# Kernel optimization log

Measured on AMD Instinct MI355X. Metric: run time of the kernel, lower is better.

Reference implementation:

```python
import jax, jax.numpy as jnp
import numpy as np

N_NODES = 100000
N_EDGES = 1600000
NFEAT = 128
NHID = 128
NCLASS = 40


def gcn_conv(x, W, b, src, dst, n_nodes):
    """PyG-style GCNConv: x' = D^{-1/2}(A+I)D^{-1/2} (x W) + b."""
    h = x @ W  # [N, out]
    loop = jnp.arange(n_nodes, dtype=src.dtype)
    s = jnp.concatenate([src, loop])  # add self-loops
    d = jnp.concatenate([dst, loop])
    deg = jax.ops.segment_sum(jnp.ones_like(s, dtype=h.dtype), d, num_segments=n_nodes)
    dinv = jnp.where(deg > 0, jax.lax.rsqrt(deg), 0.0)
    norm = dinv[s] * dinv[d]  # [E+N]
    msg = h[s] * norm[:, None]  # gather + scale
    out = jax.ops.segment_sum(msg, d, num_segments=n_nodes)  # scatter-add
    return out + b


def setup_inputs() -> dict:
    key = jax.random.key(0)
    ks = jax.random.split(key, 6)
    x = jax.random.normal(ks[0], (N_NODES, NFEAT), dtype=jnp.float32)
    edge_index = jax.random.randint(ks[1], (2, N_EDGES), 0, N_NODES, dtype=jnp.int64)
    sc1 = 1.0 / np.sqrt(NFEAT)
    sc2 = 1.0 / np.sqrt(NHID)
    W1 = jax.random.normal(ks[2], (NFEAT, NHID), dtype=jnp.float32) * sc1
    b1 = jnp.zeros((NHID,), dtype=jnp.float32)
    Wm = jax.random.normal(ks[3], (NHID, NHID), dtype=jnp.float32) * sc2
    bm = jnp.zeros((NHID,), dtype=jnp.float32)
    W2 = jax.random.normal(ks[4], (NHID, NCLASS), dtype=jnp.float32) * sc2
    b2 = jnp.zeros((NCLASS,), dtype=jnp.float32)
    return {"x": x, "edge_index": edge_index, "W1": W1, "b1": b1,
            "Wm": Wm, "bm": bm, "W2": W2, "b2": b2}


def reference(x, edge_index, W1, b1, Wm, bm, W2, b2):
    # StandGCNX forward, eval mode (dropout = identity)
    src, dst = edge_index[0], edge_index[1]
    n = x.shape[0]
    h = jax.nn.relu(gcn_conv(x, W1, b1, src, dst, n))
    h = jax.nn.relu(gcn_conv(h, Wm, bm, src, dst, n))
    out = gcn_conv(h, W2, b2, src, dst, n)
    return out
```

## Files before the change

kernel.cpp:

```cpp
#include <hip/hip_runtime.h>
#include <hip/hip_bf16.h>

typedef __attribute__((ext_vector_type(8))) short bf16x8;
typedef __attribute__((ext_vector_type(4))) float f32x4;

__device__ __forceinline__ ushort bf16rne(float f) {
    uint u = __float_as_uint(f);
    return (ushort)((u + 0x7fffu + ((u >> 16) & 1u)) >> 16);
}
__device__ __forceinline__ void unpack2(uint p, float& a, float& b) {
    a = __uint_as_float(p << 16);
    b = __uint_as_float(p & 0xffff0000u);
}


__global__ __launch_bounds__(256) void k_pre1(const float* __restrict__ W1,
                                              const float* __restrict__ Wm,
                                              const float* __restrict__ W2,
                                              ushort* __restrict__ w1t,
                                              ushort* __restrict__ wmt,
                                              ushort* __restrict__ w2t,
                                              const int* __restrict__ dst,
                                              int* __restrict__ bcnt, int E) {
    __shared__ int hist[512];
    int b = blockIdx.x;
    int t = threadIdx.x;
    if (b < 152) {
        if (b < 64) {
            int i = b * 256 + t; int k = i >> 7, n = i & 127;
            w1t[n * 128 + k] = bf16rne(W1[k * 128 + n]);
        } else if (b < 128) {
            int i = (b - 64) * 256 + t; int k = i >> 7, n = i & 127;
            wmt[n * 128 + k] = bf16rne(Wm[k * 128 + n]);
        } else {
            int i = (b - 128) * 256 + t;
            if (i < 6144) {
                int n = i >> 7, k = i & 127;
                w2t[n * 128 + k] = (n < 40) ? bf16rne(W2[k * 40 + n]) : (ushort)0;
            }
        }
        return;
    }
    hist[t] = 0; hist[t + 256] = 0;
    __syncthreads();
    int off = (b - 152) * 4096;
    int cnt = min(4096, E - off);
    for (int i = t; i < cnt; i += 256) atomicAdd(&hist[dst[off + i] >> 8], 1);
    __syncthreads();
    if (hist[t]) atomicAdd(&bcnt[t], hist[t]);
    if (hist[t + 256]) atomicAdd(&bcnt[t + 256], hist[t + 256]);
}

__global__ void k_bscan(const int* __restrict__ bcnt, int* __restrict__ bbase,
                        int* __restrict__ bcur, int nbuck) {
    __shared__ int s[512];
    int t = threadIdx.x;
    s[t] = (t < nbuck) ? bcnt[t] : 0;
    __syncthreads();
    for (int d = 1; d < 512; d <<= 1) {
        int u = (t >= d) ? s[t - d] : 0;
        __syncthreads();
        if (t >= d) s[t] += u;
        __syncthreads();
    }
    int excl = (t == 0) ? 0 : s[t - 1];
    bbase[t] = excl;
    if (t < nbuck) bcur[t] = excl;
    if (t == 511) bbase[512] = s[511];
}


__global__ __launch_bounds__(256) void k_pack_gemm(const int* __restrict__ src,
                                                   const int* __restrict__ dst,
                                                   int* __restrict__ bcur,
                                                   uint* __restrict__ pairbuf,
                                                   int E, int nbuck, int ntile,
                                                   const float* __restrict__ A,
                                                   const ushort* __restrict__ Wt,
                                                   ushort* __restrict__ C, int M) {
    __shared__ int hist[512];
    __shared__ int scn[512];
    __shared__ int cur[512];
    __shared__ int gbase[512];
    __shared__ uint sorted[4096];
    int t = threadIdx.x;
    if ((int)blockIdx.x >= ntile) {
        int blk = blockIdx.x - ntile;
        int wave = t >> 6, lane = t & 63;
        int m16 = lane & 15, quad = lane >> 4;
        int rowA = blk * 64 + wave * 16 + m16;
        int rA = min(rowA, M - 1);
        const float4* A4 = (const float4*)A;

        f32x4 acc[8];
#pragma unroll
        for (int i = 0; i < 8; i++) acc[i] = (f32x4){0.f, 0.f, 0.f, 0.f};
#pragma unroll
        for (int it = 0; it < 4; it++) {
            float4 f0 = A4[(size_t)rA * 32 + 8 * it + 2 * quad];
            float4 f1 = A4[(size_t)rA * 32 + 8 * it + 2 * quad + 1];
            bf16x8 af;
            af[0] = (short)bf16rne(f0.x); af[1] = (short)bf16rne(f0.y);
            af[2] = (short)bf16rne(f0.z); af[3] = (short)bf16rne(f0.w);
            af[4] = (short)bf16rne(f1.x); af[5] = (short)bf16rne(f1.y);
            af[6] = (short)bf16rne(f1.z); af[7] = (short)bf16rne(f1.w);
#pragma unroll
            for (int nt = 0; nt < 8; nt++) {
                bf16x8 bfr = *(const bf16x8*)(Wt + (size_t)(nt * 16 + m16) * 128 + it * 32 + quad * 8);
                acc[nt] = __builtin_amdgcn_mfma_f32_16x16x32_bf16(af, bfr, acc[nt], 0, 0, 0);
            }
        }
        int rowBase = blk * 64 + wave * 16 + quad * 4;
#pragma unroll
        for (int nt = 0; nt < 8; nt++) {
            int col = nt * 16 + m16;
#pragma unroll
            for (int r = 0; r < 4; r++) {
                int row = rowBase + r;
                if (row < M) C[(size_t)row * 128 + col] = bf16rne(acc[nt][r]);
            }
        }
        return;
    }
    int off = blockIdx.x * 4096;
    int cnt = min(4096, E - off);
    hist[t] = 0; hist[t + 256] = 0;
    __syncthreads();
    for (int i = t; i < cnt; i += 256) {
        int b = dst[off + i] >> 8;
        atomicAdd(&hist[b], 1);
    }
    __syncthreads();
    scn[t] = hist[t]; scn[t + 256] = hist[t + 256];
    __syncthreads();
    for (int d = 1; d < 256; d <<= 1) {
        int u0 = (t >= d) ? scn[t - d] : 0;
        int u1 = (t >= d) ? scn[256 + t - d] : 0;
        __syncthreads();
        if (t >= d) { scn[t] += u0; scn[256 + t] += u1; }
        __syncthreads();
    }
    int tot0 = scn[255];
    scn[256 + t] += tot0;
    __syncthreads();
    cur[t] = (t == 0) ? 0 : scn[t - 1];
    cur[t + 256] = scn[t + 255];
    if (t < nbuck && hist[t] > 0) gbase[t] = atomicAdd(&bcur[t], hist[t]);
    int t2 = t + 256;
    if (t2 < nbuck && hist[t2] > 0) gbase[t2] = atomicAdd(&bcur[t2], hist[t2]);
    __syncthreads();
    for (int i = t; i < cnt; i += 256) {
        int d = dst[off + i];
        int s = src[off + i];
        int b = d >> 8;
        int pos = atomicAdd(&cur[b], 1);
        sorted[pos] = ((uint)(d & 255) << 24) | (uint)s;
    }
    __syncthreads();
    int wid = t >> 6, lane = t & 63;
    for (int b = wid; b < nbuck; b += 4) {
        int n = hist[b];
        if (n == 0) continue;
        int ls = (b == 0) ? 0 : scn[b - 1];
        int gb = gbase[b];
        for (int j = lane; j < n; j += 64)
            pairbuf[gb + j] = sorted[ls + j];
    }
}

#define CSR_CAP 5632
__global__ __launch_bounds__(256) void k_csrbuild(const uint* __restrict__ pairbuf,
                                                  const int* __restrict__ bbase,
                                                  int* __restrict__ rowptr,
                                                  float* __restrict__ dinv,
                                                  int* __restrict__ csr,
                                                  int N, int nbuck) {
    __shared__ int lhist[256];
    __shared__ int scn[256];
    __shared__ int lcur[256];
    __shared__ int lcsr[CSR_CAP];
    int b = blockIdx.x;
    int base = b << 8;
    int nn = min(256, N - base);
    int lo = bbase[b], hi = bbase[b + 1];
    int cnt = hi - lo;
    int t = threadIdx.x;
    lhist[t] = 0;
    __syncthreads();
    for (int i = t; i < cnt; i += 256) atomicAdd(&lhist[pairbuf[lo + i] >> 24], 1);
    __syncthreads();
    int mydeg = lhist[t];
    scn[t] = mydeg;
    __syncthreads();
    for (int d = 1; d < 256; d <<= 1) {
        int u = (t >= d) ? scn[t - d] : 0;
        __syncthreads();
        if (t >= d) scn[t] += u;
        __syncthreads();
    }
    int excl = (t == 0) ? 0 : scn[t - 1];
    lcur[t] = excl;
    if (t < nn) {
        rowptr[base + t] = lo + excl;
        dinv[base + t] = rsqrtf((float)(mydeg + 1));
    }
    if (b == nbuck - 1 && t == 0) rowptr[N] = hi;
    __syncthreads();
    if (cnt <= CSR_CAP) {
        for (int i = t; i < cnt; i += 256) {
            uint p = pairbuf[lo + i];
            int pos = atomicAdd(&lcur[p >> 24], 1);
            lcsr[pos] = (int)(p & 0xFFFFFFu);
        }
        __syncthreads();
        for (int i = t; i < cnt; i += 256) csr[lo + i] = lcsr[i];
    } else {
        for (int i = t; i < cnt; i += 256) {
            uint p = pairbuf[lo + i];
            int pos = lo + atomicAdd(&lcur[p >> 24], 1);
            csr[pos] = (int)(p & 0xFFFFFFu);
        }
    }
}


template <int NT, bool EDGE_W>
__device__ __forceinline__ void fused_agg_gemm(const ushort* __restrict__ g,
                                               const float* __restrict__ dinv,
                                               const int* __restrict__ rowptr,
                                               const int* __restrict__ csr,
                                               const float* __restrict__ bias,
                                               const ushort* __restrict__ Wt,
                                               ushort* __restrict__ C,
                                               int M, int ccols) {
    __shared__ ushort hs[32][136];
    __shared__ int nextNode;
    int t = threadIdx.x;
    if (t == 0) nextNode = 0;
    int l = t & 15;
    const uint4* g16 = (const uint4*)g;
    float4 bb0 = ((const float4*)bias)[2 * l];
    float4 bb1 = ((const float4*)bias)[2 * l + 1];
    __syncthreads();

    for (;;) {
        int idx = 0;
        if (l == 0) idx = atomicAdd(&nextNode, 1);
        idx = __shfl(idx, (t & 63) & ~15, 64);
        if (idx >= 32) break;
        int node = blockIdx.x * 32 + idx;
        int nd = min(node, M - 1);
        float dn = dinv[nd];
        float a[8];
        {
            uint4 p = g16[(size_t)nd * 16 + l];
            float u, v;
            if (EDGE_W) {
                unpack2(p.x, u, v); a[0] = u * dn; a[1] = v * dn;
                unpack2(p.y, u, v); a[2] = u * dn; a[3] = v * dn;
                unpack2(p.z, u, v); a[4] = u * dn; a[5] = v * dn;
                unpack2(p.w, u, v); a[6] = u * dn; a[7] = v * dn;
            } else {
                unpack2(p.x, a[0], a[1]); unpack2(p.y, a[2], a[3]);
                unpack2(p.z, a[4], a[5]); unpack2(p.w, a[6], a[7]);
            }
        }
        int e0 = rowptr[nd], e1 = rowptr[nd + 1];
        int e = e0;
        for (; e + 4 <= e1; e += 4) {
            int s0 = csr[e], s1 = csr[e + 1], s2 = csr[e + 2], s3 = csr[e + 3];
            float w0 = 1.f, w1 = 1.f, w2 = 1.f, w3 = 1.f;
            if (EDGE_W) { w0 = dinv[s0]; w1 = dinv[s1]; w2 = dinv[s2]; w3 = dinv[s3]; }
            uint4 p0 = g16[(size_t)s0 * 16 + l];
            uint4 p1 = g16[(size_t)s1 * 16 + l];
            uint4 p2 = g16[(size_t)s2 * 16 + l];
            uint4 p3 = g16[(size_t)s3 * 16 + l];
            float u, v;
            if (EDGE_W) {
                unpack2(p0.x, u, v); a[0] += u * w0; a[1] += v * w0;
                unpack2(p0.y, u, v); a[2] += u * w0; a[3] += v * w0;
                unpack2(p0.z, u, v); a[4] += u * w0; a[5] += v * w0;
                unpack2(p0.w, u, v); a[6] += u * w0; a[7] += v * w0;
                unpack2(p1.x, u, v); a[0] += u * w1; a[1] += v * w1;
                unpack2(p1.y, u, v); a[2] += u * w1; a[3] += v * w1;
                unpack2(p1.z, u, v); a[4] += u * w1; a[5] += v * w1;
                unpack2(p1.w, u, v); a[6] += u * w1; a[7] += v * w1;
                unpack2(p2.x, u, v); a[0] += u * w2; a[1] += v * w2;
                unpack2(p2.y, u, v); a[2] += u * w2; a[3] += v * w2;
                unpack2(p2.z, u, v); a[4] += u * w2; a[5] += v * w2;
                unpack2(p2.w, u, v); a[6] += u * w2; a[7] += v * w2;
                unpack2(p3.x, u, v); a[0] += u * w3; a[1] += v * w3;
                unpack2(p3.y, u, v); a[2] += u * w3; a[3] += v * w3;
                unpack2(p3.z, u, v); a[4] += u * w3; a[5] += v * w3;
                unpack2(p3.w, u, v); a[6] += u * w3; a[7] += v * w3;
            } else {
                unpack2(p0.x, u, v); a[0] += u; a[1] += v;
                unpack2(p0.y, u, v); a[2] += u; a[3] += v;
                unpack2(p0.z, u, v); a[4] += u; a[5] += v;
                unpack2(p0.w, u, v); a[6] += u; a[7] += v;
                unpack2(p1.x, u, v); a[0] += u; a[1] += v;
                unpack2(p1.y, u, v); a[2] += u; a[3] += v;
                unpack2(p1.z, u, v); a[4] += u; a[5] += v;
                unpack2(p1.w, u, v); a[6] += u; a[7] += v;
                unpack2(p2.x, u, v); a[0] += u; a[1] += v;
                unpack2(p2.y, u, v); a[2] += u; a[3] += v;
                unpack2(p2.z, u, v); a[4] += u; a[5] += v;
                unpack2(p2.w, u, v); a[6] += u; a[7] += v;
                unpack2(p3.x, u, v); a[0] += u; a[1] += v;
                unpack2(p3.y, u, v); a[2] += u; a[3] += v;
                unpack2(p3.z, u, v); a[4] += u; a[5] += v;
                unpack2(p3.w, u, v); a[6] += u; a[7] += v;
            }
        }
        for (; e < e1; e++) {
            int s = csr[e];
            float w = EDGE_W ? dinv[s] : 1.f;
            uint4 p = g16[(size_t)s * 16 + l];
            float u, v;
            unpack2(p.x, u, v); a[0] += u * w; a[1] += v * w;
            unpack2(p.y, u, v); a[2] += u * w; a[3] += v * w;
            unpack2(p.z, u, v); a[4] += u * w; a[5] += v * w;
            unpack2(p.w, u, v); a[6] += u * w; a[7] += v * w;
        }
        float o0 = fmaxf(a[0] * dn + bb0.x, 0.f);
        float o1 = fmaxf(a[1] * dn + bb0.y, 0.f);
        float o2 = fmaxf(a[2] * dn + bb0.z, 0.f);
        float o3 = fmaxf(a[3] * dn + bb0.w, 0.f);
        float o4 = fmaxf(a[4] * dn + bb1.x, 0.f);
        float o5 = fmaxf(a[5] * dn + bb1.y, 0.f);
        float o6 = fmaxf(a[6] * dn + bb1.z, 0.f);
        float o7 = fmaxf(a[7] * dn + bb1.w, 0.f);
        uint4 qv;
        qv.x = (uint)bf16rne(o0) | ((uint)bf16rne(o1) << 16);
        qv.y = (uint)bf16rne(o2) | ((uint)bf16rne(o3) << 16);
        qv.z = (uint)bf16rne(o4) | ((uint)bf16rne(o5) << 16);
        qv.w = (uint)bf16rne(o6) | ((uint)bf16rne(o7) << 16);
        *(uint4*)&hs[idx][l * 8] = qv;
    }
    __syncthreads();

    int wave = t >> 6, lane = t & 63;
    int m16 = lane & 15, quad = lane >> 4;
    int rowHalf = wave & 1;
    int ntHalf = wave >> 1;
    constexpr int NTH = (NT + 1) / 2;
    int ntStart = ntHalf * NTH;
    int ntEnd = ntHalf ? NT : NTH;

    f32x4 acc[NTH];
#pragma unroll
    for (int i = 0; i < NTH; i++) acc[i] = (f32x4){0.f, 0.f, 0.f, 0.f};
#pragma unroll
    for (int it = 0; it < 4; it++) {
        bf16x8 af = *(const bf16x8*)&hs[rowHalf * 16 + m16][it * 32 + quad * 8];
        for (int nt = ntStart; nt < ntEnd; nt++) {
            bf16x8 bfr = *(const bf16x8*)(Wt + (size_t)(nt * 16 + m16) * 128 + it * 32 + quad * 8);
            acc[nt - ntStart] = __builtin_amdgcn_mfma_f32_16x16x32_bf16(af, bfr, acc[nt - ntStart], 0, 0, 0);
        }
    }
    int rowBase = blockIdx.x * 32 + rowHalf * 16 + quad * 4;
    float dnv[4];
#pragma unroll
    for (int r = 0; r < 4; r++) dnv[r] = dinv[min(rowBase + r, M - 1)];
    for (int nt = ntStart; nt < ntEnd; nt++) {
        int col = nt * 16 + m16;
        if (col >= ccols) continue;
#pragma unroll
        for (int r = 0; r < 4; r++) {
            int row = rowBase + r;
            if (row < M) C[(size_t)row * ccols + col] = bf16rne(acc[nt - ntStart][r] * dnv[r]);
        }
    }
}

__global__ __launch_bounds__(256) void k_fusedA(const ushort* __restrict__ g,
                                                const float* __restrict__ dinv,
                                                const int* __restrict__ rowptr,
                                                const int* __restrict__ csr,
                                                const float* __restrict__ bias,
                                                const ushort* __restrict__ Wt,
                                                ushort* __restrict__ C, int M) {
    fused_agg_gemm<8, true>(g, dinv, rowptr, csr, bias, Wt, C, M, 128);
}

__global__ __launch_bounds__(256) void k_fusedB(const ushort* __restrict__ g,
                                                const float* __restrict__ dinv,
                                                const int* __restrict__ rowptr,
                                                const int* __restrict__ csr,
                                                const float* __restrict__ bias,
                                                const ushort* __restrict__ Wt,
                                                ushort* __restrict__ C, int M) {
    fused_agg_gemm<3, false>(g, dinv, rowptr, csr, bias, Wt, C, M, 40);
}


__global__ __launch_bounds__(256) void k_agg40_b(const ushort* __restrict__ g3,
                                                 const float* __restrict__ dinv,
                                                 const int* __restrict__ rowptr,
                                                 const int* __restrict__ csr,
                                                 const float* __restrict__ bias,
                                                 float* __restrict__ out, int N) {
    int t = threadIdx.x;
    if (t >= 250) return;
    int grp = t / 10;
    int l = t - grp * 10;
    int node = blockIdx.x * 25 + grp;
    if (node >= N) return;
    const uint2* gp = (const uint2*)g3;
    float dn = dinv[node];
    float a0, a1, a2, a3;
    {
        uint2 p = gp[(size_t)node * 10 + l];
        unpack2(p.x, a0, a1);
        unpack2(p.y, a2, a3);
    }
    int e0 = rowptr[node], e1 = rowptr[node + 1];
    int e = e0;
    for (; e + 4 <= e1; e += 4) {
        int s0 = csr[e], s1 = csr[e + 1], s2 = csr[e + 2], s3 = csr[e + 3];
        uint2 p0 = gp[(size_t)s0 * 10 + l];
        uint2 p1 = gp[(size_t)s1 * 10 + l];
        uint2 p2 = gp[(size_t)s2 * 10 + l];
        uint2 p3 = gp[(size_t)s3 * 10 + l];
        float u, v;
        unpack2(p0.x, u, v); a0 += u; a1 += v;
        unpack2(p0.y, u, v); a2 += u; a3 += v;
        unpack2(p1.x, u, v); a0 += u; a1 += v;
        unpack2(p1.y, u, v); a2 += u; a3 += v;
        unpack2(p2.x, u, v); a0 += u; a1 += v;
        unpack2(p2.y, u, v); a2 += u; a3 += v;
        unpack2(p3.x, u, v); a0 += u; a1 += v;
        unpack2(p3.y, u, v); a2 += u; a3 += v;
    }
    for (; e < e1; e++) {
        int s = csr[e];
        uint2 p = gp[(size_t)s * 10 + l];
        float u, v;
        unpack2(p.x, u, v); a0 += u; a1 += v;
        unpack2(p.y, u, v); a2 += u; a3 += v;
    }
    float4 bb = ((const float4*)bias)[l];
    float4 o;
    o.x = a0 * dn + bb.x;
    o.y = a1 * dn + bb.y;
    o.z = a2 * dn + bb.z;
    o.w = a3 * dn + bb.w;
    ((float4*)out)[(size_t)node * 10 + l] = o;
}


extern "C" void kernel_launch(void* const* d_in, const int* in_sizes, int n_in,
                              void* d_out, int out_size, void* d_ws, size_t ws_size,
                              hipStream_t stream) {
    const float* x  = (const float*)d_in[0];
    const int* eidx = (const int*)d_in[1];
    const float* W1 = (const float*)d_in[2];
    const float* b1 = (const float*)d_in[3];
    const float* Wm = (const float*)d_in[4];
    const float* bm = (const float*)d_in[5];
    const float* W2 = (const float*)d_in[6];
    const float* b2 = (const float*)d_in[7];
    float* out = (float*)d_out;

    int N = in_sizes[0] / 128;
    int E = in_sizes[1] / 2;
    const int* src = eidx;
    const int* dst = eidx + E;
    int nbuck = (N + 255) >> 8;
    int ntile = (E + 4095) / 4096;

    char* ws = (char*)d_ws;
    size_t off = 0;
    auto alloc = [&](size_t bytes) -> void* {
        void* p = ws + off;
        off += (bytes + 255) & ~(size_t)255;
        return p;
    };
    float*  dinv    = (float*)alloc((size_t)N * 4);
    int*    rowptr  = (int*)alloc(((size_t)N + 1) * 4);
    int*    csr     = (int*)alloc((size_t)E * 4);
    uint*   pairbuf = (uint*)alloc((size_t)E * 4);
    int*    bcnt    = (int*)alloc(512 * 4);
    int*    bbase   = (int*)alloc(513 * 4);
    int*    bcur    = (int*)alloc(512 * 4);
    ushort* w1t     = (ushort*)alloc(128 * 128 * 2);
    ushort* wmt     = (ushort*)alloc(128 * 128 * 2);
    ushort* w2t     = (ushort*)alloc(48 * 128 * 2);
    ushort* gbuf    = (ushort*)alloc((size_t)N * 128 * 2);
    ushort* gbuf2   = (ushort*)alloc((size_t)N * 128 * 2);
    ushort* g3      = (ushort*)alloc((size_t)N * 40 * 2);

    int gblk64 = (N + 63) / 64;
    int gblk32 = (N + 31) / 32;

    hipMemsetAsync(bcnt, 0, 512 * 4, stream);
    k_pre1<<<152 + ntile, 256, 0, stream>>>(W1, Wm, W2, w1t, wmt, w2t, dst, bcnt, E);
    k_bscan<<<1, 512, 0, stream>>>(bcnt, bbase, bcur, nbuck);
    k_pack_gemm<<<ntile + gblk64, 256, 0, stream>>>(src, dst, bcur, pairbuf, E, nbuck,
                                                    ntile, x, w1t, gbuf, N);
    k_csrbuild<<<nbuck, 256, 0, stream>>>(pairbuf, bbase, rowptr, dinv, csr, N, nbuck);
    k_fusedA<<<gblk32, 256, 0, stream>>>(gbuf, dinv, rowptr, csr, b1, wmt, gbuf2, N);
    k_fusedB<<<gblk32, 256, 0, stream>>>(gbuf2, dinv, rowptr, csr, bm, w2t, g3, N);
    k_agg40_b<<<(N + 24) / 25, 256, 0, stream>>>(g3, dinv, rowptr, csr, b2, out, N);
}
```

Measured before the change: 368.3 us.

## Split fused aggregation+GEMM kernels into separate aggregation and MFMA GEMM kernels

Replaces the two fused aggregate-then-GEMM kernels with four kernels. Two are plain per-node gather aggregations writing a bf16 hidden buffer, and two are standalone MFMA GEMMs that read that buffer. This removes the LDS staging, the atomic work-stealing loop and the block-wide sync that tied aggregation to the GEMM, and allows simpler, higher-occupancy kernels. The cost is an extra 25.6MB bf16 intermediate written and read twice, plus two more kernel launches.

```diff
diff --git a/kernel.cpp b/kernel.cpp
--- a/kernel.cpp
+++ b/kernel.cpp
@@ -224,173 +224,176 @@
 }
 
 
-template <int NT, bool EDGE_W>
-__device__ __forceinline__ void fused_agg_gemm(const ushort* __restrict__ g,
-                                               const float* __restrict__ dinv,
-                                               const int* __restrict__ rowptr,
-                                               const int* __restrict__ csr,
-                                               const float* __restrict__ bias,
-                                               const ushort* __restrict__ Wt,
-                                               ushort* __restrict__ C,
-                                               int M, int ccols) {
-    __shared__ ushort hs[32][136];
-    __shared__ int nextNode;
-    int t = threadIdx.x;
-    if (t == 0) nextNode = 0;
+template <bool EDGE_W>
+__device__ __forceinline__ void agg128_body(const ushort* __restrict__ g,
+                                            const float* __restrict__ dinv,
+                                            const int* __restrict__ rowptr,
+                                            const int* __restrict__ csr,
+                                            const float* __restrict__ bias,
+                                            ushort* __restrict__ hout, int N) {
+    int t = threadIdx.x;
+    int grp = t >> 4;
     int l = t & 15;
+    int node = blockIdx.x * 16 + grp;
+    if (node >= N) return;
     const uint4* g16 = (const uint4*)g;
-    float4 bb0 = ((const float4*)bias)[2 * l];
-    float4 bb1 = ((const float4*)bias)[2 * l + 1];
-    __syncthreads();
-
-    for (;;) {
-        int idx = 0;
-        if (l == 0) idx = atomicAdd(&nextNode, 1);
-        idx = __shfl(idx, (t & 63) & ~15, 64);
-        if (idx >= 32) break;
-        int node = blockIdx.x * 32 + idx;
-        int nd = min(node, M - 1);
-        float dn = dinv[nd];
-        float a[8];
-        {
-            uint4 p = g16[(size_t)nd * 16 + l];
-            float u, v;
-            if (EDGE_W) {
-                unpack2(p.x, u, v); a[0] = u * dn; a[1] = v * dn;
-                unpack2(p.y, u, v); a[2] = u * dn; a[3] = v * dn;
-                unpack2(p.z, u, v); a[4] = u * dn; a[5] = v * dn;
-                unpack2(p.w, u, v); a[6] = u * dn; a[7] = v * dn;
-            } else {
-                unpack2(p.x, a[0], a[1]); unpack2(p.y, a[2], a[3]);
-                unpack2(p.z, a[4], a[5]); unpack2(p.w, a[6], a[7]);
-            }
-        }
-        int e0 = rowptr[nd], e1 = rowptr[nd + 1];
-        int e = e0;
-        for (; e + 4 <= e1; e += 4) {
-            int s0 = csr[e], s1 = csr[e + 1], s2 = csr[e + 2], s3 = csr[e + 3];
-            float w0 = 1.f, w1 = 1.f, w2 = 1.f, w3 = 1.f;
-            if (EDGE_W) { w0 = dinv[s0]; w1 = dinv[s1]; w2 = dinv[s2]; w3 = dinv[s3]; }
-            uint4 p0 = g16[(size_t)s0 * 16 + l];
-            uint4 p1 = g16[(size_t)s1 * 16 + l];
-            uint4 p2 = g16[(size_t)s2 * 16 + l];
-            uint4 p3 = g16[(size_t)s3 * 16 + l];
-            float u, v;
-            if (EDGE_W) {
-                unpack2(p0.x, u, v); a[0] += u * w0; a[1] += v * w0;
-                unpack2(p0.y, u, v); a[2] += u * w0; a[3] += v * w0;
-                unpack2(p0.z, u, v); a[4] += u * w0; a[5] += v * w0;
-                unpack2(p0.w, u, v); a[6] += u * w0; a[7] += v * w0;
-                unpack2(p1.x, u, v); a[0] += u * w1; a[1] += v * w1;
-                unpack2(p1.y, u, v); a[2] += u * w1; a[3] += v * w1;
-                unpack2(p1.z, u, v); a[4] += u * w1; a[5] += v * w1;
-                unpack2(p1.w, u, v); a[6] += u * w1; a[7] += v * w1;
-                unpack2(p2.x, u, v); a[0] += u * w2; a[1] += v * w2;
-                unpack2(p2.y, u, v); a[2] += u * w2; a[3] += v * w2;
-                unpack2(p2.z, u, v); a[4] += u * w2; a[5] += v * w2;
-                unpack2(p2.w, u, v); a[6] += u * w2; a[7] += v * w2;
-                unpack2(p3.x, u, v); a[0] += u * w3; a[1] += v * w3;
-                unpack2(p3.y, u, v); a[2] += u * w3; a[3] += v * w3;
-                unpack2(p3.z, u, v); a[4] += u * w3; a[5] += v * w3;
-                unpack2(p3.w, u, v); a[6] += u * w3; a[7] += v * w3;
-            } else {
-                unpack2(p0.x, u, v); a[0] += u; a[1] += v;
-                unpack2(p0.y, u, v); a[2] += u; a[3] += v;
-                unpack2(p0.z, u, v); a[4] += u; a[5] += v;
-                unpack2(p0.w, u, v); a[6] += u; a[7] += v;
-                unpack2(p1.x, u, v); a[0] += u; a[1] += v;
-                unpack2(p1.y, u, v); a[2] += u; a[3] += v;
-                unpack2(p1.z, u, v); a[4] += u; a[5] += v;
-                unpack2(p1.w, u, v); a[6] += u; a[7] += v;
-                unpack2(p2.x, u, v); a[0] += u; a[1] += v;
-                unpack2(p2.y, u, v); a[2] += u; a[3] += v;
-                unpack2(p2.z, u, v); a[4] += u; a[5] += v;
-                unpack2(p2.w, u, v); a[6] += u; a[7] += v;
-                unpack2(p3.x, u, v); a[0] += u; a[1] += v;
-                unpack2(p3.y, u, v); a[2] += u; a[3] += v;
-                unpack2(p3.z, u, v); a[4] += u; a[5] += v;
-                unpack2(p3.w, u, v); a[6] += u; a[7] += v;
-            }
-        }
-        for (; e < e1; e++) {
-            int s = csr[e];
-            float w = EDGE_W ? dinv[s] : 1.f;
-            uint4 p = g16[(size_t)s * 16 + l];
-            float u, v;
-            unpack2(p.x, u, v); a[0] += u * w; a[1] += v * w;
-            unpack2(p.y, u, v); a[2] += u * w; a[3] += v * w;
-            unpack2(p.z, u, v); a[4] += u * w; a[5] += v * w;
-            unpack2(p.w, u, v); a[6] += u * w; a[7] += v * w;
-        }
-        float o0 = fmaxf(a[0] * dn + bb0.x, 0.f);
-        float o1 = fmaxf(a[1] * dn + bb0.y, 0.f);
-        float o2 = fmaxf(a[2] * dn + bb0.z, 0.f);
-        float o3 = fmaxf(a[3] * dn + bb0.w, 0.f);
-        float o4 = fmaxf(a[4] * dn + bb1.x, 0.f);
-        float o5 = fmaxf(a[5] * dn + bb1.y, 0.f);
-        float o6 = fmaxf(a[6] * dn + bb1.z, 0.f);
-        float o7 = fmaxf(a[7] * dn + bb1.w, 0.f);
-        uint4 qv;
-        qv.x = (uint)bf16rne(o0) | ((uint)bf16rne(o1) << 16);
-        qv.y = (uint)bf16rne(o2) | ((uint)bf16rne(o3) << 16);
-        qv.z = (uint)bf16rne(o4) | ((uint)bf16rne(o5) << 16);
-        qv.w = (uint)bf16rne(o6) | ((uint)bf16rne(o7) << 16);
-        *(uint4*)&hs[idx][l * 8] = qv;
-    }
-    __syncthreads();
-
+    float dn = dinv[node];
+    float a[8];
+    {
+        uint4 p = g16[(size_t)node * 16 + l];
+        float u, v;
+        if (EDGE_W) {
+            unpack2(p.x, u, v); a[0] = u * dn; a[1] = v * dn;
+            unpack2(p.y, u, v); a[2] = u * dn; a[3] = v * dn;
+            unpack2(p.z, u, v); a[4] = u * dn; a[5] = v * dn;
+            unpack2(p.w, u, v); a[6] = u * dn; a[7] = v * dn;
+        } else {
+            unpack2(p.x, a[0], a[1]); unpack2(p.y, a[2], a[3]);
+            unpack2(p.z, a[4], a[5]); unpack2(p.w, a[6], a[7]);
+        }
+    }
+    int e0 = rowptr[node], e1 = rowptr[node + 1];
+    int e = e0;
+    for (; e + 4 <= e1; e += 4) {
+        int s0 = csr[e], s1 = csr[e + 1], s2 = csr[e + 2], s3 = csr[e + 3];
+        float w0 = 1.f, w1 = 1.f, w2 = 1.f, w3 = 1.f;
+        if (EDGE_W) { w0 = dinv[s0]; w1 = dinv[s1]; w2 = dinv[s2]; w3 = dinv[s3]; }
+        uint4 p0 = g16[(size_t)s0 * 16 + l];
+        uint4 p1 = g16[(size_t)s1 * 16 + l];
+        uint4 p2 = g16[(size_t)s2 * 16 + l];
+        uint4 p3 = g16[(size_t)s3 * 16 + l];
+        float u, v;
+        if (EDGE_W) {
+            unpack2(p0.x, u, v); a[0] += u * w0; a[1] += v * w0;
+            unpack2(p0.y, u, v); a[2] += u * w0; a[3] += v * w0;
+            unpack2(p0.z, u, v); a[4] += u * w0; a[5] += v * w0;
+            unpack2(p0.w, u, v); a[6] += u * w0; a[7] += v * w0;
+            unpack2(p1.x, u, v); a[0] += u * w1; a[1] += v * w1;
+            unpack2(p1.y, u, v); a[2] += u * w1; a[3] += v * w1;
+            unpack2(p1.z, u, v); a[4] += u * w1; a[5] += v * w1;
+            unpack2(p1.w, u, v); a[6] += u * w1; a[7] += v * w1;
+            unpack2(p2.x, u, v); a[0] += u * w2; a[1] += v * w2;
+            unpack2(p2.y, u, v); a[2] += u * w2; a[3] += v * w2;
+            unpack2(p2.z, u, v); a[4] += u * w2; a[5] += v * w2;
+            unpack2(p2.w, u, v); a[6] += u * w2; a[7] += v * w2;
+            unpack2(p3.x, u, v); a[0] += u * w3; a[1] += v * w3;
+            unpack2(p3.y, u, v); a[2] += u * w3; a[3] += v * w3;
+            unpack2(p3.z, u, v); a[4] += u * w3; a[5] += v * w3;
+            unpack2(p3.w, u, v); a[6] += u * w3; a[7] += v * w3;
+        } else {
+            unpack2(p0.x, u, v); a[0] += u; a[1] += v;
+            unpack2(p0.y, u, v); a[2] += u; a[3] += v;
+            unpack2(p0.z, u, v); a[4] += u; a[5] += v;
+            unpack2(p0.w, u, v); a[6] += u; a[7] += v;
+            unpack2(p1.x, u, v); a[0] += u; a[1] += v;
+            unpack2(p1.y, u, v); a[2] += u; a[3] += v;
+            unpack2(p1.z, u, v); a[4] += u; a[5] += v;
+            unpack2(p1.w, u, v); a[6] += u; a[7] += v;
+            unpack2(p2.x, u, v); a[0] += u; a[1] += v;
+            unpack2(p2.y, u, v); a[2] += u; a[3] += v;
+            unpack2(p2.z, u, v); a[4] += u; a[5] += v;
+            unpack2(p2.w, u, v); a[6] += u; a[7] += v;
+            unpack2(p3.x, u, v); a[0] += u; a[1] += v;
+            unpack2(p3.y, u, v); a[2] += u; a[3] += v;
+            unpack2(p3.z, u, v); a[4] += u; a[5] += v;
+            unpack2(p3.w, u, v); a[6] += u; a[7] += v;
+        }
+    }
+    for (; e < e1; e++) {
+        int s = csr[e];
+        float w = EDGE_W ? dinv[s] : 1.f;
+        uint4 p = g16[(size_t)s * 16 + l];
+        float u, v;
+        unpack2(p.x, u, v); a[0] += u * w; a[1] += v * w;
+        unpack2(p.y, u, v); a[2] += u * w; a[3] += v * w;
+        unpack2(p.z, u, v); a[4] += u * w; a[5] += v * w;
+        unpack2(p.w, u, v); a[6] += u * w; a[7] += v * w;
+    }
+    float4 b0 = ((const float4*)bias)[2 * l];
+    float4 b1 = ((const float4*)bias)[2 * l + 1];
+    float o[8];
+    o[0] = fmaxf(a[0] * dn + b0.x, 0.f); o[1] = fmaxf(a[1] * dn + b0.y, 0.f);
+    o[2] = fmaxf(a[2] * dn + b0.z, 0.f); o[3] = fmaxf(a[3] * dn + b0.w, 0.f);
+    o[4] = fmaxf(a[4] * dn + b1.x, 0.f); o[5] = fmaxf(a[5] * dn + b1.y, 0.f);
+    o[6] = fmaxf(a[6] * dn + b1.z, 0.f); o[7] = fmaxf(a[7] * dn + b1.w, 0.f);
+    uint4 q;
+    q.x = (uint)bf16rne(o[0]) | ((uint)bf16rne(o[1]) << 16);
+    q.y = (uint)bf16rne(o[2]) | ((uint)bf16rne(o[3]) << 16);
+    q.z = (uint)bf16rne(o[4]) | ((uint)bf16rne(o[5]) << 16);
+    q.w = (uint)bf16rne(o[6]) | ((uint)bf16rne(o[7]) << 16);
+    ((uint4*)hout)[(size_t)node * 16 + l] = q;
+}
+
+__global__ __launch_bounds__(256) void k_aggA(const ushort* __restrict__ g,
+                                              const float* __restrict__ dinv,
+                                              const int* __restrict__ rowptr,
+                                              const int* __restrict__ csr,
+                                              const float* __restrict__ bias,
+                                              ushort* __restrict__ hout, int N) {
+    agg128_body<true>(g, dinv, rowptr, csr, bias, hout, N);
+}
+
+__global__ __launch_bounds__(256) void k_aggB(const ushort* __restrict__ g,
+                                              const float* __restrict__ dinv,
+                                              const int* __restrict__ rowptr,
+                                              const int* __restrict__ csr,
+                                              const float* __restrict__ bias,
+                                              ushort* __restrict__ hout, int N) {
+    agg128_body<false>(g, dinv, rowptr, csr, bias, hout, N);
+}
+
+
+template <int NT>
+__device__ __forceinline__ void gemm_body(const ushort* __restrict__ A,
+                                          const ushort* __restrict__ Wt,
+                                          const float* __restrict__ dinv,
+                                          ushort* __restrict__ C, int M, int ccols) {
+    int t = threadIdx.x;
     int wave = t >> 6, lane = t & 63;
     int m16 = lane & 15, quad = lane >> 4;
-    int rowHalf = wave & 1;
-    int ntHalf = wave >> 1;
-    constexpr int NTH = (NT + 1) / 2;
-    int ntStart = ntHalf * NTH;
-    int ntEnd = ntHalf ? NT : NTH;
-
-    f32x4 acc[NTH];
-#pragma unroll
-    for (int i = 0; i < NTH; i++) acc[i] = (f32x4){0.f, 0.f, 0.f, 0.f};
+    int rowA = blockIdx.x * 64 + wave * 16 + m16;
+    int rA = min(rowA, M - 1);
+
+    f32x4 acc[NT];
+#pragma unroll
+    for (int i = 0; i < NT; i++) acc[i] = (f32x4){0.f, 0.f, 0.f, 0.f};
 #pragma unroll
     for (int it = 0; it < 4; it++) {
-        bf16x8 af = *(const bf16x8*)&hs[rowHalf * 16 + m16][it * 32 + quad * 8];
-        for (int nt = ntStart; nt < ntEnd; nt++) {
+        bf16x8 af = *(const bf16x8*)(A + (size_t)rA * 128 + it * 32 + quad * 8);
+#pragma unroll
+        for (int nt = 0; nt < NT; nt++) {
             bf16x8 bfr = *(const bf16x8*)(Wt + (size_t)(nt * 16 + m16) * 128 + it * 32 + quad * 8);
-            acc[nt - ntStart] = __builtin_amdgcn_mfma_f32_16x16x32_bf16(af, bfr, acc[nt - ntStart], 0, 0, 0);
-        }
-    }
-    int rowBase = blockIdx.x * 32 + rowHalf * 16 + quad * 4;
+            acc[nt] = __builtin_amdgcn_mfma_f32_16x16x32_bf16(af, bfr, acc[nt], 0, 0, 0);
+        }
+    }
+    int rowBase = blockIdx.x * 64 + wave * 16 + quad * 4;
     float dnv[4];
 #pragma unroll
     for (int r = 0; r < 4; r++) dnv[r] = dinv[min(rowBase + r, M - 1)];
-    for (int nt = ntStart; nt < ntEnd; nt++) {
+#pragma unroll
+    for (int nt = 0; nt < NT; nt++) {
         int col = nt * 16 + m16;
         if (col >= ccols) continue;
 #pragma unroll
         for (int r = 0; r < 4; r++) {
             int row = rowBase + r;
-            if (row < M) C[(size_t)row * ccols + col] = bf16rne(acc[nt - ntStart][r] * dnv[r]);
-        }
-    }
-}
-
-__global__ __launch_bounds__(256) void k_fusedA(const ushort* __restrict__ g,
-                                                const float* __restrict__ dinv,
-                                                const int* __restrict__ rowptr,
-                                                const int* __restrict__ csr,
-                                                const float* __restrict__ bias,
-                                                const ushort* __restrict__ Wt,
-                                                ushort* __restrict__ C, int M) {
-    fused_agg_gemm<8, true>(g, dinv, rowptr, csr, bias, Wt, C, M, 128);
-}
-
-__global__ __launch_bounds__(256) void k_fusedB(const ushort* __restrict__ g,
-                                                const float* __restrict__ dinv,
-                                                const int* __restrict__ rowptr,
-                                                const int* __restrict__ csr,
-                                                const float* __restrict__ bias,
-                                                const ushort* __restrict__ Wt,
-                                                ushort* __restrict__ C, int M) {
-    fused_agg_gemm<3, false>(g, dinv, rowptr, csr, bias, Wt, C, M, 40);
+            if (row < M) C[(size_t)row * ccols + col] = bf16rne(acc[nt][r] * dnv[r]);
+        }
+    }
+}
+
+__global__ __launch_bounds__(256) void k_gemm128s(const ushort* __restrict__ A,
+                                                  const ushort* __restrict__ Wt,
+                                                  const float* __restrict__ dinv,
+                                                  ushort* __restrict__ C, int M) {
+    gemm_body<8>(A, Wt, dinv, C, M, 128);
+}
+
+__global__ __launch_bounds__(256) void k_gemm40s(const ushort* __restrict__ A,
+                                                 const ushort* __restrict__ Wt,
+                                                 const float* __restrict__ dinv,
+                                                 ushort* __restrict__ C, int M) {
+    gemm_body<3>(A, Wt, dinv, C, M, 40);
 }
 
 
@@ -487,11 +490,12 @@
     ushort* wmt     = (ushort*)alloc(128 * 128 * 2);
     ushort* w2t     = (ushort*)alloc(48 * 128 * 2);
     ushort* gbuf    = (ushort*)alloc((size_t)N * 128 * 2);
+    ushort* hbuf    = (ushort*)alloc((size_t)N * 128 * 2);
     ushort* gbuf2   = (ushort*)alloc((size_t)N * 128 * 2);
     ushort* g3      = (ushort*)alloc((size_t)N * 40 * 2);
 
     int gblk64 = (N + 63) / 64;
-    int gblk32 = (N + 31) / 32;
+    int gblk16 = (N + 15) / 16;
 
     hipMemsetAsync(bcnt, 0, 512 * 4, stream);
     k_pre1<<<152 + ntile, 256, 0, stream>>>(W1, Wm, W2, w1t, wmt, w2t, dst, bcnt, E);
@@ -499,7 +503,9 @@
     k_pack_gemm<<<ntile + gblk64, 256, 0, stream>>>(src, dst, bcur, pairbuf, E, nbuck,
                                                     ntile, x, w1t, gbuf, N);
     k_csrbuild<<<nbuck, 256, 0, stream>>>(pairbuf, bbase, rowptr, dinv, csr, N, nbuck);
-    k_fusedA<<<gblk32, 256, 0, stream>>>(gbuf, dinv, rowptr, csr, b1, wmt, gbuf2, N);
-    k_fusedB<<<gblk32, 256, 0, stream>>>(gbuf2, dinv, rowptr, csr, bm, w2t, g3, N);
+    k_aggA<<<gblk16, 256, 0, stream>>>(gbuf, dinv, rowptr, csr, b1, hbuf, N);
+    k_gemm128s<<<gblk64, 256, 0, stream>>>(hbuf, wmt, dinv, gbuf2, N);
+    k_aggB<<<gblk16, 256, 0, stream>>>(gbuf2, dinv, rowptr, csr, bm, hbuf, N);
+    k_gemm40s<<<gblk64, 256, 0, stream>>>(hbuf, w2t, dinv, g3, N);
     k_agg40_b<<<(N + 24) / 25, 256, 0, stream>>>(g3, dinv, rowptr, csr, b2, out, N);
 }
```

New measurement: 386.6 us. +4.9%, slower.
